# Kernel optimization log

Hardware: AMD Instinct MI355X
Metric: run time of the kernel (lower is better)

## Reference

```python
import jax, jax.numpy as jnp
import numpy as np

N_FEATURES = 1024
N_HEADS = 16
D_ATTN = 64


def setup_inputs() -> dict:
    key = jax.random.key(0)
    k_x, k_qkv, k_pw, k_pb = jax.random.split(key, 4)
    B, S = 2, 2048
    x = jax.random.normal(k_x, (B, S, N_FEATURES), dtype=jnp.float32)
    # torch nn.Linear weights are [out, in]; init scale ~ 1/sqrt(in)
    w_qkv = jax.random.normal(k_qkv, (3 * N_HEADS * D_ATTN, N_FEATURES), dtype=jnp.float32) / np.sqrt(N_FEATURES)
    w_proj = jax.random.normal(k_pw, (N_FEATURES, N_HEADS * D_ATTN), dtype=jnp.float32) / np.sqrt(N_HEADS * D_ATTN)
    b_proj = jax.random.normal(k_pb, (N_FEATURES,), dtype=jnp.float32) / np.sqrt(N_HEADS * D_ATTN)
    return {"x": x, "w_qkv": w_qkv, "w_proj": w_proj, "b_proj": b_proj}


def reference(x, w_qkv, w_proj, b_proj):
    B, S, F = x.shape
    H, D = N_HEADS, D_ATTN
    # fused QKV projection (bias=False): [B,S,3*H*D]
    qkv = jnp.einsum('bsf,of->bso', x, w_qkv)
    qkv = qkv.reshape(B, S, 3, H, D)
    q = jnp.transpose(qkv[:, :, 0], (0, 2, 1, 3))  # [B,H,S,D]
    k = jnp.transpose(qkv[:, :, 1], (0, 2, 1, 3))
    v = jnp.transpose(qkv[:, :, 2], (0, 2, 1, 3))
    scale = 1.0 / jnp.sqrt(jnp.asarray(D, dtype=x.dtype))
    scores = jnp.einsum('bhqd,bhkd->bhqk', q, k) * scale  # [B,H,S,S]
    attn = jax.nn.softmax(scores, axis=-1)
    out = jnp.einsum('bhqk,bhkd->bhqd', attn, v)  # [B,H,S,D]
    out = jnp.transpose(out, (0, 2, 1, 3)).reshape(B, S, H * D)
    # output projection (dropout is identity in eval mode)
    return jnp.einsum('bsm,fm->bsf', out, w_proj) + b_proj
```

## Files before the change

kernel.cpp:

```cpp
#include <hip/hip_runtime.h>
#include <hip/hip_bf16.h>
#include <math.h>

#define BATCH 2
#define SEQ 2048
#define NFEAT 1024
#define NHEAD 16
#define DHEAD 64
#define MROWS (BATCH * SEQ)
#define NQKV (3 * NHEAD * DHEAD)

typedef __attribute__((ext_vector_type(8))) short short8;
typedef __attribute__((ext_vector_type(4))) float floatx4;

#define CEXP 0.18033688f

__device__ __forceinline__ unsigned short f2bf(float f) {
    unsigned int u = __float_as_uint(f);
    u += 0x7fff + ((u >> 16) & 1);
    return (unsigned short)(u >> 16);
}

__device__ __forceinline__ float fast_exp2(float x) {
    return __builtin_amdgcn_exp2f(x);
}

__device__ __forceinline__ uint pack_bf16x2(float lo, float hi) {
    float2 t; t.x = lo; t.y = hi;
    __hip_bfloat162 h = __float22bfloat162_rn(t);
    union { __hip_bfloat162 h; uint u; } c; c.h = h;
    return c.u;
}

__device__ __forceinline__ void async16(const void* g, void* l) {
    __builtin_amdgcn_global_load_lds(
        (const __attribute__((address_space(1))) void*)g,
        (__attribute__((address_space(3))) void*)l, 16, 0, 0);
}

__global__ void cvt_swz(const float* __restrict__ x, const float* __restrict__ wq,
                        const float* __restrict__ wp,
                        ushort* __restrict__ xb, ushort* __restrict__ wqb,
                        ushort* __restrict__ wpb) {
    const int NX = MROWS * NFEAT / 4, NWQ = NQKV * NFEAT / 4, NWP = NFEAT * NFEAT / 4;
    int i = blockIdx.x * blockDim.x + threadIdx.x;
    if (i >= NX + NWQ + NWP) return;
    const float* src; ushort* dst; int idx4;
    if (i < NX)            { src = x;  dst = xb;  idx4 = i; }
    else if (i < NX + NWQ) { src = wq; dst = wqb; idx4 = i - NX; }
    else                   { src = wp; dst = wpb; idx4 = i - NX - NWQ; }
    float4 v = ((const float4*)src)[idx4];
    ushort4 o;
    o.x = f2bf(v.x); o.y = f2bf(v.y); o.z = f2bf(v.z); o.w = f2bf(v.w);
    const int e = idx4 * 4;
    const int k = e & (NFEAT - 1);
    const int row = e >> 10;
    const int kp = (k & ~31) | (((((k >> 3) & 3) ^ ((row >> 1) & 3))) << 3) | (k & 7);
    *(ushort4*)(dst + (size_t)row * NFEAT + kp) = o;
}

__global__ __launch_bounds__(256, 3)
void gemm_qkv(const ushort* __restrict__ A, const ushort* __restrict__ W,
              ushort* __restrict__ qb, ushort* __restrict__ kb, ushort* __restrict__ vtb) {
    __shared__ ushort smem[16384];
    ushort* As = smem;
    ushort* Bs = smem + 8192;
    const int tid = threadIdx.x;
    const int wave = tid >> 6, lane = tid & 63;
    const int id = blockIdx.x;
    const int xcd = id & 7, slot = id >> 3;
    const int by = (xcd >> 1) * 8 + slot / 12;
    const int bx = (xcd & 1) * 12 + slot % 12;
    const int m0 = by * 128, n0 = bx * 128;
    const int wm = (wave >> 1) * 64, wn = (wave & 1) * 64;
    const int lr = lane & 15, lg = lane >> 4;
    const int kswz = (lg ^ ((lr >> 1) & 3)) * 8;

    floatx4 acc[4][4] = {};

    for (int k0 = 0; k0 < NFEAT; k0 += 64) {
#pragma unroll
        for (int q = 0; q < 4; ++q) {
            const int s = q * 256 + tid;
            const int row = s >> 3, kc = (s & 7) * 8;
            async16(A + (size_t)(m0 + row) * NFEAT + k0 + kc, (void*)(As + s * 8));
            async16(W + (size_t)(n0 + row) * NFEAT + k0 + kc, (void*)(Bs + s * 8));
        }
        __syncthreads();
#pragma unroll
        for (int kk = 0; kk < 2; ++kk) {
            short8 a[4], b[4];
#pragma unroll
            for (int i = 0; i < 4; ++i)
                a[i] = *(const short8*)(As + (wm + i * 16 + lr) * 64 + kk * 32 + kswz);
#pragma unroll
            for (int j = 0; j < 4; ++j)
                b[j] = *(const short8*)(Bs + (wn + j * 16 + lr) * 64 + kk * 32 + kswz);
#pragma unroll
            for (int i = 0; i < 4; ++i)
#pragma unroll
                for (int j = 0; j < 4; ++j)
                    acc[i][j] = __builtin_amdgcn_mfma_f32_16x16x32_bf16(a[i], b[j], acc[i][j], 0, 0, 0);
        }
        __syncthreads();
    }

    const int t = n0 >> 10;
    const int bidx = m0 >> 11;
    if (t < 2) {
#pragma unroll
        for (int i = 0; i < 4; ++i)
#pragma unroll
            for (int j = 0; j < 4; ++j)
#pragma unroll
                for (int r = 0; r < 4; ++r) {
                    const int m = m0 + wm + i * 16 + lg * 4 + r;
                    const int n = n0 + wn + j * 16 + lr;
                    const int s = m & (SEQ - 1);
                    const int rem = n & 1023, h = rem >> 6, d = rem & 63;
                    if (t == 0) {
                        qb[((size_t)(bidx * NHEAD + h) * SEQ + s) * DHEAD + d] =
                            f2bf(acc[i][j][r] * CEXP);
                    } else {
                        const int dcol = ((((d >> 3) ^ (s & 7)) << 3)) | (d & 7);
                        kb[((size_t)(bidx * NHEAD + h) * SEQ + s) * DHEAD + dcol] =
                            f2bf(acc[i][j][r]);
                    }
                }
    } else {
#pragma unroll
        for (int hhalf = 0; hhalf < 2; ++hhalf) {
            if ((wm >> 6) == hhalf) {
#pragma unroll
                for (int i = 0; i < 4; ++i) {
                    const int chunk = i * 2 + (lg >> 1);
#pragma unroll
                    for (int j = 0; j < 4; ++j) {
                        const int n = wn + j * 16 + lr;
                        uint2 pk;
                        pk.x = pack_bf16x2(acc[i][j][0], acc[i][j][1]);
                        pk.y = pack_bf16x2(acc[i][j][2], acc[i][j][3]);
                        *(uint2*)(smem + n * 64 + ((chunk ^ (n & 7)) * 8) + (lg & 1) * 4) = pk;
                    }
                }
            }
            __syncthreads();
            const int s_base = (m0 & (SEQ - 1)) + hhalf * 64;
#pragma unroll
            for (int it = 0; it < 4; ++it) {
                const int n_r = (tid >> 3) + it * 32;
                const int p = tid & 7;
                short8 rowv = *(const short8*)(smem + n_r * 64 + p * 8);
                const int nglob = n0 + n_r;
                const int d = nglob & 63, hh = (nglob & 1023) >> 6;
                *(short8*)(vtb + ((size_t)(bidx * NHEAD + hh) * DHEAD + d) * SEQ + s_base + p * 8) = rowv;
            }
            __syncthreads();
        }
    }
}

__global__ __launch_bounds__(256, 2)
void gemm_proj(const ushort* __restrict__ A, const ushort* __restrict__ W,
               const float* __restrict__ bias, float* __restrict__ Cout) {
    __shared__ ushort As[128 * 64];
    __shared__ ushort Bs[64 * 64];
    const int tid = threadIdx.x;
    const int wave = tid >> 6, lane = tid & 63;
    const int id = blockIdx.x;
    const int xcd = id & 7, slot = id >> 3;
    const int by = (xcd >> 1) * 8 + (slot >> 3);
    const int bx = (xcd & 1) * 8 + (slot & 7);
    const int m0 = by * 128, n0 = bx * 64;
    const int wm = (wave >> 1) * 64, wn = (wave & 1) * 32;
    const int lr = lane & 15, lg = lane >> 4;
    const int kswz = (lg ^ ((lr >> 1) & 3)) * 8;

    floatx4 acc[4][2] = {};

    for (int k0 = 0; k0 < NFEAT; k0 += 64) {
#pragma unroll
        for (int q = 0; q < 4; ++q) {
            const int s = q * 256 + tid;
            const int row = s >> 3, kc = (s & 7) * 8;
            async16(A + (size_t)(m0 + row) * NFEAT + k0 + kc, (void*)(As + s * 8));
        }
#pragma unroll
        for (int q = 0; q < 2; ++q) {
            const int s = q * 256 + tid;
            const int row = s >> 3, kc = (s & 7) * 8;
            async16(W + (size_t)(n0 + row) * NFEAT + k0 + kc, (void*)(Bs + s * 8));
        }
        __syncthreads();
#pragma unroll
        for (int kk = 0; kk < 2; ++kk) {
            short8 a[4], b[2];
#pragma unroll
            for (int i = 0; i < 4; ++i)
                a[i] = *(const short8*)(As + (wm + i * 16 + lr) * 64 + kk * 32 + kswz);
#pragma unroll
            for (int j = 0; j < 2; ++j)
                b[j] = *(const short8*)(Bs + (wn + j * 16 + lr) * 64 + kk * 32 + kswz);
#pragma unroll
            for (int i = 0; i < 4; ++i)
#pragma unroll
                for (int j = 0; j < 2; ++j)
                    acc[i][j] = __builtin_amdgcn_mfma_f32_16x16x32_bf16(a[i], b[j], acc[i][j], 0, 0, 0);
        }
        __syncthreads();
    }

#pragma unroll
    for (int i = 0; i < 4; ++i)
#pragma unroll
        for (int j = 0; j < 2; ++j)
#pragma unroll
            for (int r = 0; r < 4; ++r) {
                const int m = m0 + wm + i * 16 + lg * 4 + r;
                const int n = n0 + wn + j * 16 + lr;
                Cout[(size_t)m * NFEAT + n] = acc[i][j][r] + bias[n];
            }
}

__global__ __launch_bounds__(256, 2)
void flash_attn(const ushort* __restrict__ qb, const ushort* __restrict__ kb,
                const ushort* __restrict__ vtb, ushort* __restrict__ aob) {
    const int id = blockIdx.x;
    const int xcd = id & 7, slot = id >> 3;
    const int bh = xcd + 8 * (slot >> 4);
    const int qt = slot & 15;
    const int tid = threadIdx.x, wave = tid >> 6, lane = tid & 63;
    const int lr = lane & 15, lg = lane >> 4;

    __shared__ ushort Ks[2][64 * 64];
    __shared__ ushort Vs[2][64 * 64];
    __shared__ ushort Ps_all[4][32 * 64];
    ushort* Ps = Ps_all[wave];

    const ushort* Qb = qb + (size_t)bh * SEQ * DHEAD;
    const ushort* Kb = kb + (size_t)bh * SEQ * DHEAD;
    const ushort* Vt = vtb + (size_t)bh * DHEAD * SEQ;

    const int q0 = qt * 128 + wave * 32;

    short8 qf[2][2];
#pragma unroll
    for (int j = 0; j < 2; ++j)
#pragma unroll
        for (int kk = 0; kk < 2; ++kk)
            qf[j][kk] = *(const short8*)(Qb + (size_t)(q0 + j * 16 + lr) * DHEAD + kk * 32 + lg * 8);

    const int kofs = tid * 8;
    const size_t vrow = (size_t)(tid >> 3) * SEQ;
    const int vcol = (tid & 7) * 8;

    async16(Kb + kofs,                    (void*)(Ks[0] + kofs));
    async16(Kb + 2048 + kofs,             (void*)(Ks[0] + 2048 + kofs));
    async16(Vt + vrow + vcol,             (void*)(Vs[0] + kofs));
    async16(Vt + 32 * SEQ + vrow + vcol,  (void*)(Vs[0] + 2048 + kofs));

    floatx4 acc_o[2][4] = {};
    float l_lane[2] = {0.0f, 0.0f};
    const int sw = lr & 7;

#define FLASH_PREFETCH(BUF, KV)                                                     \
    {                                                                               \
        const int kv_ = (KV);                                                       \
        async16(Kb + (size_t)kv_ * DHEAD + kofs,          (void*)(Ks[BUF] + kofs)); \
        async16(Kb + (size_t)kv_ * DHEAD + 2048 + kofs,   (void*)(Ks[BUF] + 2048 + kofs)); \
        async16(Vt + vrow + kv_ + vcol,                   (void*)(Vs[BUF] + kofs)); \
        async16(Vt + 32 * SEQ + vrow + kv_ + vcol,        (void*)(Vs[BUF] + 2048 + kofs)); \
    }

#define FLASH_COMPUTE(BUF)                                                          \
    {                                                                               \
        floatx4 st[4][2] = {};                                                      \
        _Pragma("unroll")                                                           \
        for (int kk = 0; kk < 2; ++kk)                                              \
            _Pragma("unroll")                                                       \
            for (int i = 0; i < 4; ++i) {                                           \
                short8 kf = *(const short8*)(Ks[BUF] + (i * 16 + lr) * 64 +         \
                                             (((kk * 4 + lg) ^ sw) * 8));           \
                _Pragma("unroll")                                                   \
                for (int j = 0; j < 2; ++j)                                         \
                    st[i][j] = __builtin_amdgcn_mfma_f32_16x16x32_bf16(kf, qf[j][kk], st[i][j], 0, 0, 0); \
            }                                                                       \
        _Pragma("unroll")                                                           \
        for (int i = 0; i < 4; ++i)                                                 \
            _Pragma("unroll")                                                       \
            for (int j = 0; j < 2; ++j) {                                           \
                const float p0 = fast_exp2(st[i][j][0]);                            \
                const float p1 = fast_exp2(st[i][j][1]);                            \
                const float p2 = fast_exp2(st[i][j][2]);                            \
                const float p3 = fast_exp2(st[i][j][3]);                            \
                l_lane[j] += (p0 + p1) + (p2 + p3);                                 \
                uint2 pk;                                                           \
                pk.x = pack_bf16x2(p0, p1);                                         \
                pk.y = pack_bf16x2(p2, p3);                                         \
                const int chunk = i * 2 + (lg >> 1);                                \
                *(uint2*)(Ps + (j * 16 + lr) * 64 + ((chunk ^ sw) * 8) + (lg & 1) * 4) = pk; \
            }                                                                       \
        _Pragma("unroll")                                                           \
        for (int kk2 = 0; kk2 < 2; ++kk2) {                                         \
            short8 vf[4];                                                           \
            _Pragma("unroll")                                                       \
            for (int j2 = 0; j2 < 4; ++j2)                                          \
                vf[j2] = *(const short8*)(Vs[BUF] + (j2 * 16 + lr) * 64 +           \
                                          (((kk2 * 4 + lg) ^ sw) * 8));             \
            _Pragma("unroll")                                                       \
            for (int i2 = 0; i2 < 2; ++i2) {                                        \
                short8 pf = *(const short8*)(Ps + (i2 * 16 + lr) * 64 +             \
                                             (((kk2 * 4 + lg) ^ sw) * 8));          \
                _Pragma("unroll")                                                   \
                for (int j2 = 0; j2 < 4; ++j2)                                      \
                    acc_o[i2][j2] = __builtin_amdgcn_mfma_f32_16x16x32_bf16(pf, vf[j2], acc_o[i2][j2], 0, 0, 0); \
            }                                                                       \
        }                                                                           \
    }

    for (int kt = 0; kt < SEQ / 64; kt += 2) {
        __syncthreads();
        FLASH_PREFETCH(1, (kt + 1) * 64)
        FLASH_COMPUTE(0)
        __syncthreads();
        if (kt + 2 < SEQ / 64)
            FLASH_PREFETCH(0, (kt + 2) * 64)
        FLASH_COMPUTE(1)
    }
#undef FLASH_PREFETCH
#undef FLASH_COMPUTE

#pragma unroll
    for (int j = 0; j < 2; ++j) {
        l_lane[j] += __shfl_xor(l_lane[j], 16);
        l_lane[j] += __shfl_xor(l_lane[j], 32);
    }

    const int b = bh >> 4, h = bh & 15;
#pragma unroll
    for (int i2 = 0; i2 < 2; ++i2) {
#pragma unroll
        for (int r = 0; r < 4; ++r) {
            const float lq = __shfl(l_lane[i2], lg * 4 + r);
            const float invl = 1.0f / lq;
            const int srow = b * SEQ + q0 + i2 * 16 + lg * 4 + r;
            const int key = (srow >> 1) & 3;
#pragma unroll
            for (int j2 = 0; j2 < 4; ++j2) {
                const int d = j2 * 16 + lr;
                const int dsw = (d & ~31) | (((((d >> 3) & 3) ^ key)) << 3) | (d & 7);
                aob[(size_t)srow * (NHEAD * DHEAD) + h * DHEAD + dsw] = f2bf(acc_o[i2][j2][r] * invl);
            }
        }
    }
}

extern "C" void kernel_launch(void* const* d_in, const int* in_sizes, int n_in,
                              void* d_out, int out_size, void* d_ws, size_t ws_size,
                              hipStream_t stream) {
    const float* x      = (const float*)d_in[0];
    const float* w_qkv  = (const float*)d_in[1];
    const float* w_proj = (const float*)d_in[2];
    const float* b_proj = (const float*)d_in[3];
    float* out = (float*)d_out;

    ushort* ws = (ushort*)d_ws;
    ushort* xb     = ws;
    ushort* wqkvb  = xb + (size_t)MROWS * NFEAT;
    ushort* wprojb = wqkvb + (size_t)NQKV * NFEAT;
    ushort* qb     = wprojb + (size_t)NFEAT * NFEAT;
    ushort* kb     = qb + (size_t)MROWS * NFEAT;
    ushort* vtb    = kb + (size_t)MROWS * NFEAT;
    ushort* aob    = vtb + (size_t)MROWS * NFEAT;

    {
        const int total = (MROWS * NFEAT + NQKV * NFEAT + NFEAT * NFEAT) / 4;
        cvt_swz<<<(total + 255) / 256, 256, 0, stream>>>(x, w_qkv, w_proj, xb, wqkvb, wprojb);
    }

    {
        gemm_qkv<<<768, 256, 0, stream>>>(xb, wqkvb, qb, kb, vtb);
    }

    {
        flash_attn<<<512, 256, 0, stream>>>(qb, kb, vtb, aob);
    }

    {
        gemm_proj<<<512, 256, 0, stream>>>(aob, wprojb, b_proj, out);
    }
}
```

Baseline: 181.9 us.

## Switch flash attention to 32x32x16 MFMA with in-register P via permlane32 swap

```diff
diff --git a/kernel.cpp b/kernel.cpp
--- a/kernel.cpp
+++ b/kernel.cpp
@@ -12,6 +12,8 @@
 
 typedef __attribute__((ext_vector_type(8))) short short8;
 typedef __attribute__((ext_vector_type(4))) float floatx4;
+typedef __attribute__((ext_vector_type(16))) float floatx16;
+typedef __attribute__((ext_vector_type(4))) unsigned int uintx4;
 
 #define CEXP 0.18033688f
 
@@ -230,12 +232,11 @@
     const int bh = xcd + 8 * (slot >> 4);
     const int qt = slot & 15;
     const int tid = threadIdx.x, wave = tid >> 6, lane = tid & 63;
-    const int lr = lane & 15, lg = lane >> 4;
+    const int l31 = lane & 31, l5 = lane >> 5;
+    const int swz = lane & 7;
 
     __shared__ ushort Ks[2][64 * 64];
     __shared__ ushort Vs[2][64 * 64];
-    __shared__ ushort Ps_all[4][32 * 64];
-    ushort* Ps = Ps_all[wave];
 
     const ushort* Qb = qb + (size_t)bh * SEQ * DHEAD;
     const ushort* Kb = kb + (size_t)bh * SEQ * DHEAD;
@@ -243,12 +244,10 @@
 
     const int q0 = qt * 128 + wave * 32;
 
-    short8 qf[2][2];
-#pragma unroll
-    for (int j = 0; j < 2; ++j)
-#pragma unroll
-        for (int kk = 0; kk < 2; ++kk)
-            qf[j][kk] = *(const short8*)(Qb + (size_t)(q0 + j * 16 + lr) * DHEAD + kk * 32 + lg * 8);
+    short8 qf[4];
+#pragma unroll
+    for (int kw = 0; kw < 4; ++kw)
+        qf[kw] = *(const short8*)(Qb + (size_t)(q0 + l31) * DHEAD + kw * 16 + l5 * 8);
 
     const int kofs = tid * 8;
     const size_t vrow = (size_t)(tid >> 3) * SEQ;
@@ -259,9 +258,8 @@
     async16(Vt + vrow + vcol,             (void*)(Vs[0] + kofs));
     async16(Vt + 32 * SEQ + vrow + vcol,  (void*)(Vs[0] + 2048 + kofs));
 
-    floatx4 acc_o[2][4] = {};
-    float l_lane[2] = {0.0f, 0.0f};
-    const int sw = lr & 7;
+    floatx16 acc_o[2] = {};
+    float l_lane = 0.0f;
 
 #define FLASH_PREFETCH(BUF, KV)                                                     \
     {                                                                               \
@@ -274,48 +272,53 @@
 
 #define FLASH_COMPUTE(BUF)                                                          \
     {                                                                               \
-        floatx4 st[4][2] = {};                                                      \
+        floatx16 st[2] = {};                                                        \
+        __builtin_amdgcn_s_setprio(1);                                              \
         _Pragma("unroll")                                                           \
-        for (int kk = 0; kk < 2; ++kk)                                              \
+        for (int kw = 0; kw < 4; ++kw) {                                            \
             _Pragma("unroll")                                                       \
-            for (int i = 0; i < 4; ++i) {                                           \
-                short8 kf = *(const short8*)(Ks[BUF] + (i * 16 + lr) * 64 +         \
-                                             (((kk * 4 + lg) ^ sw) * 8));           \
-                _Pragma("unroll")                                                   \
-                for (int j = 0; j < 2; ++j)                                         \
-                    st[i][j] = __builtin_amdgcn_mfma_f32_16x16x32_bf16(kf, qf[j][kk], st[i][j], 0, 0, 0); \
-            }                                                                       \
-        _Pragma("unroll")                                                           \
-        for (int i = 0; i < 4; ++i)                                                 \
-            _Pragma("unroll")                                                       \
-            for (int j = 0; j < 2; ++j) {                                           \
-                const float p0 = fast_exp2(st[i][j][0]);                            \
-                const float p1 = fast_exp2(st[i][j][1]);                            \
-                const float p2 = fast_exp2(st[i][j][2]);                            \
-                const float p3 = fast_exp2(st[i][j][3]);                            \
-                l_lane[j] += (p0 + p1) + (p2 + p3);                                 \
-                uint2 pk;                                                           \
-                pk.x = pack_bf16x2(p0, p1);                                         \
-                pk.y = pack_bf16x2(p2, p3);                                         \
-                const int chunk = i * 2 + (lg >> 1);                                \
-                *(uint2*)(Ps + (j * 16 + lr) * 64 + ((chunk ^ sw) * 8) + (lg & 1) * 4) = pk; \
-            }                                                                       \
-        _Pragma("unroll")                                                           \
-        for (int kk2 = 0; kk2 < 2; ++kk2) {                                         \
-            short8 vf[4];                                                           \
-            _Pragma("unroll")                                                       \
-            for (int j2 = 0; j2 < 4; ++j2)                                          \
-                vf[j2] = *(const short8*)(Vs[BUF] + (j2 * 16 + lr) * 64 +           \
-                                          (((kk2 * 4 + lg) ^ sw) * 8));             \
-            _Pragma("unroll")                                                       \
-            for (int i2 = 0; i2 < 2; ++i2) {                                        \
-                short8 pf = *(const short8*)(Ps + (i2 * 16 + lr) * 64 +             \
-                                             (((kk2 * 4 + lg) ^ sw) * 8));          \
-                _Pragma("unroll")                                                   \
-                for (int j2 = 0; j2 < 4; ++j2)                                      \
-                    acc_o[i2][j2] = __builtin_amdgcn_mfma_f32_16x16x32_bf16(pf, vf[j2], acc_o[i2][j2], 0, 0, 0); \
+            for (int i = 0; i < 2; ++i) {                                           \
+                short8 kf = *(const short8*)(Ks[BUF] + (i * 32 + l31) * 64 +        \
+                                             (((kw * 2 + l5) ^ swz) * 8));          \
+                st[i] = __builtin_amdgcn_mfma_f32_32x32x16_bf16(kf, qf[kw], st[i], 0, 0, 0); \
             }                                                                       \
         }                                                                           \
+        __builtin_amdgcn_s_setprio(0);                                              \
+        uintx4 pa[4];                                                               \
+        _Pragma("unroll")                                                           \
+        for (int i = 0; i < 2; ++i) {                                               \
+            uint P2[8];                                                             \
+            _Pragma("unroll")                                                       \
+            for (int rr = 0; rr < 8; ++rr) {                                        \
+                const float p0 = fast_exp2(st[i][rr * 2]);                          \
+                const float p1 = fast_exp2(st[i][rr * 2 + 1]);                      \
+                l_lane += p0 + p1;                                                  \
+                P2[rr] = pack_bf16x2(p0, p1);                                       \
+            }                                                                       \
+            _Pragma("unroll")                                                       \
+            for (int r3 = 0; r3 < 2; ++r3) {                                        \
+                _Pragma("unroll")                                                   \
+                for (int r1 = 0; r1 < 2; ++r1) {                                    \
+                    uint a = P2[r3 * 4 + r1];                            \
+                    uint b = P2[r3 * 4 + 2 + r1];                        \
+                    asm volatile("v_permlane32_swap_b32 %0, %1" : "+v"(a), "+v"(b)); \
+                    pa[i * 2 + r3][r1] = a;               \
+                    pa[i * 2 + r3][2 + r1] = b;           \
+                }                                                                   \
+            }                                                                       \
+        }                                                                           \
+        __builtin_amdgcn_s_setprio(1);                                              \
+        _Pragma("unroll")                                                           \
+        for (int kk = 0; kk < 4; ++kk) {                                            \
+            const short8 paf = *(const short8*)&pa[kk];                             \
+            _Pragma("unroll")                                                       \
+            for (int j2 = 0; j2 < 2; ++j2) {                                        \
+                short8 vf = *(const short8*)(Vs[BUF] + (j2 * 32 + l31) * 64 +       \
+                                             (((kk * 2 + l5) ^ swz) * 8));          \
+                acc_o[j2] = __builtin_amdgcn_mfma_f32_32x32x16_bf16(paf, vf, acc_o[j2], 0, 0, 0); \
+            }                                                                       \
+        }                                                                           \
+        __builtin_amdgcn_s_setprio(0);                                              \
     }
 
     for (int kt = 0; kt < SEQ / 64; kt += 2) {
@@ -330,27 +333,21 @@
 #undef FLASH_PREFETCH
 #undef FLASH_COMPUTE
 
-#pragma unroll
-    for (int j = 0; j < 2; ++j) {
-        l_lane[j] += __shfl_xor(l_lane[j], 16);
-        l_lane[j] += __shfl_xor(l_lane[j], 32);
-    }
+    l_lane += __shfl_xor(l_lane, 32);
+    const float invl = 1.0f / l_lane;
 
     const int b = bh >> 4, h = bh & 15;
 #pragma unroll
-    for (int i2 = 0; i2 < 2; ++i2) {
-#pragma unroll
-        for (int r = 0; r < 4; ++r) {
-            const float lq = __shfl(l_lane[i2], lg * 4 + r);
-            const float invl = 1.0f / lq;
-            const int srow = b * SEQ + q0 + i2 * 16 + lg * 4 + r;
-            const int key = (srow >> 1) & 3;
-#pragma unroll
-            for (int j2 = 0; j2 < 4; ++j2) {
-                const int d = j2 * 16 + lr;
-                const int dsw = (d & ~31) | (((((d >> 3) & 3) ^ key)) << 3) | (d & 7);
-                aob[(size_t)srow * (NHEAD * DHEAD) + h * DHEAD + dsw] = f2bf(acc_o[i2][j2][r] * invl);
-            }
+    for (int r = 0; r < 16; ++r) {
+        const int qrow = (r & 3) + 4 * l5 + 8 * (r >> 2);
+        const float il = __shfl(invl, qrow);
+        const int srow = b * SEQ + q0 + qrow;
+        const int key = (srow >> 1) & 3;
+#pragma unroll
+        for (int j2 = 0; j2 < 2; ++j2) {
+            const int d = j2 * 32 + l31;
+            const int dsw = (d & ~31) | ((((d >> 3) & 3) ^ key) << 3) | (d & 7);
+            aob[(size_t)srow * (NHEAD * DHEAD) + h * DHEAD + dsw] = f2bf(acc_o[j2][r] * il);
         }
     }
 }
```

New measurement: 176.1 us. -3.2%, faster.
